# Performance work log

Measured on AMD Instinct MI355X. Metric: run time of the kernel, lower is better.

Reference implementation:

```python
import jax, jax.numpy as jnp
import numpy as np

B, SQ, SKV, D = 16, 4096, 4096, 64

def setup_inputs() -> dict:
    key = jax.random.key(0)
    kq, kk, kv, ks = jax.random.split(key, 4)
    return {
        "q": jax.random.normal(kq, (B, SQ, D), dtype=jnp.float32),
        "k": jax.random.normal(kk, (B, SKV, D), dtype=jnp.float32),
        "v": jax.random.normal(kv, (B, SKV, D), dtype=jnp.float32),
        "scale_factor": jax.random.uniform(ks, (1,), dtype=jnp.float32, minval=0.05, maxval=0.2),
    }

def reference(q, k, v, scale_factor):
    # qk = q @ k^T, then divide by inv_scale = 1/scale  ==  multiply by scale
    scores = jnp.einsum("bqd,bkd->bqk", q, k) * scale_factor[0]  # [B, SQ, SKV]
    probs = jax.nn.softmax(scores, axis=-1)
    # dropout p=0.0 -> identity (source's p=1 would zero the output; see notes)
    out = jnp.einsum("bqk,bkd->bqd", probs, v)  # [B, SQ, D]
    return out
```

## Files before the change

### kernel.cpp

```cpp
#include <hip/hip_runtime.h>
#include <hip/hip_bf16.h>

#define BATCH 16
#define SEQ   4096
#define DH    64
#define KVB   64
#define NT    (SEQ / KVB)
#define LDK   72

using frag   = __attribute__((ext_vector_type(8))) short;
using f32x16 = __attribute__((ext_vector_type(16))) float;
using u16x8  = __attribute__((ext_vector_type(8))) unsigned short;

__device__ __forceinline__ unsigned short f2bf(float x) {
    union { __hip_bfloat16 h; unsigned short u; } cv;
    cv.h = __float2bfloat16(x);
    return cv.u;
}
__device__ __forceinline__ unsigned int pk2bf(float lo, float hi) {
    return (unsigned int)f2bf(lo) | ((unsigned int)f2bf(hi) << 16);
}
__device__ __forceinline__ float fast_exp2(float x) {
#if __has_builtin(__builtin_amdgcn_exp2f)
    return __builtin_amdgcn_exp2f(x);
#else
    float r; asm("v_exp_f32 %0, %1" : "=v"(r) : "v"(x)); return r;
#endif
}
__device__ __forceinline__ unsigned int cvtpk_bf16(float lo, float hi) {
    unsigned int r;
    asm("v_cvt_pk_bf16_f32 %0, %1, %2" : "=v"(r) : "v"(lo), "v"(hi));
    return r;
}
__device__ __forceinline__ void glds16(const unsigned short* g, unsigned short* l) {
    __builtin_amdgcn_global_load_lds(
        (const __attribute__((address_space(1))) void*)g,
        (__attribute__((address_space(3))) void*)l, 16, 0, 0);
}

__global__ __launch_bounds__(256) void cvt_k_frag(const float* __restrict__ K,
                                                  unsigned short* __restrict__ Kws) {
    __shared__ unsigned short Ls[64 * LDK];
    const int b = blockIdx.x >> 6;
    const int t = blockIdx.x & 63;
    const int i = threadIdx.x;
    {
        const int kv = i >> 2, db = (i & 3) * 16;
        const float* src = K + ((size_t)b * SEQ + (size_t)t * 64 + kv) * DH + db;
        float4 a = *(const float4*)(src);
        float4 c = *(const float4*)(src + 4);
        float4 d = *(const float4*)(src + 8);
        float4 e = *(const float4*)(src + 12);
        u16x8 w0, w1;
        w0[0]=f2bf(a.x); w0[1]=f2bf(a.y); w0[2]=f2bf(a.z); w0[3]=f2bf(a.w);
        w0[4]=f2bf(c.x); w0[5]=f2bf(c.y); w0[6]=f2bf(c.z); w0[7]=f2bf(c.w);
        w1[0]=f2bf(d.x); w1[1]=f2bf(d.y); w1[2]=f2bf(d.z); w1[3]=f2bf(d.w);
        w1[4]=f2bf(e.x); w1[5]=f2bf(e.y); w1[6]=f2bf(e.z); w1[7]=f2bf(e.w);
        *(u16x8*)&Ls[kv * LDK + db]     = w0;
        *(u16x8*)&Ls[kv * LDK + db + 8] = w1;
    }
    __syncthreads();
    {
        const int flat0 = i * 2;
        const int f     = flat0 >> 6;
        const int kb    = f & 1, kstep = f >> 1;
        const int l0    = flat0 & 63, l1 = l0 + 1;
        u16x8 o0 = *(const u16x8*)&Ls[(kb*32 + (l0&31)) * LDK + kstep*16 + (l0>>5)*8];
        u16x8 o1 = *(const u16x8*)&Ls[(kb*32 + (l1&31)) * LDK + kstep*16 + (l1>>5)*8];
        unsigned short* dst = Kws + ((((size_t)b*64 + t)*8 + f)*64 + l0)*8;
        *(u16x8*)dst       = o0;
        *(u16x8*)(dst + 8) = o1;
    }
}

__global__ __launch_bounds__(256) void tr_v_frag(const float* __restrict__ V,
                                                 unsigned short* __restrict__ Vws) {
    __shared__ unsigned short Ls[64 * LDK];
    const int b = blockIdx.x >> 6;
    const int t = blockIdx.x & 63;
    const int i = threadIdx.x;
    {
        const int kv = i >> 2, db = (i & 3) * 16;
        const float* src = V + ((size_t)b * SEQ + (size_t)t * 64 + kv) * DH + db;
        float4 a = *(const float4*)(src);
        float4 c = *(const float4*)(src + 4);
        float4 d = *(const float4*)(src + 8);
        float4 e = *(const float4*)(src + 12);
        u16x8 w0, w1;
        w0[0]=f2bf(a.x); w0[1]=f2bf(a.y); w0[2]=f2bf(a.z); w0[3]=f2bf(a.w);
        w0[4]=f2bf(c.x); w0[5]=f2bf(c.y); w0[6]=f2bf(c.z); w0[7]=f2bf(c.w);
        w1[0]=f2bf(d.x); w1[1]=f2bf(d.y); w1[2]=f2bf(d.z); w1[3]=f2bf(d.w);
        w1[4]=f2bf(e.x); w1[5]=f2bf(e.y); w1[6]=f2bf(e.z); w1[7]=f2bf(e.w);
        *(u16x8*)&Ls[kv * LDK + db]     = w0;
        *(u16x8*)&Ls[kv * LDK + db + 8] = w1;
    }
    __syncthreads();
    {
        const int flat0 = i * 2;
        const int fv    = flat0 >> 6;
        const int kb    = fv >> 2, ks = (fv >> 1) & 1, dblk = fv & 1;
        u16x8 o0, o1;
        const int l0 = flat0 & 63, l1 = l0 + 1;
#pragma unroll
        for (int j = 0; j < 8; ++j)
            o0[j] = Ls[(kb*32 + ks*16 + (l0>>5)*8 + j) * LDK + dblk*32 + (l0&31)];
#pragma unroll
        for (int j = 0; j < 8; ++j)
            o1[j] = Ls[(kb*32 + ks*16 + (l1>>5)*8 + j) * LDK + dblk*32 + (l1&31)];
        unsigned short* dst = Vws + ((((size_t)b*64 + t)*8 + fv)*64 + l0)*8;
        *(u16x8*)dst       = o0;
        *(u16x8*)(dst + 8) = o1;
    }
}

__global__ __launch_bounds__(128, 2) void attn_fwd(
    const float* __restrict__ Q, const unsigned short* __restrict__ Kws,
    const unsigned short* __restrict__ Vws, const float* __restrict__ S,
    float* __restrict__ O)
{
    __shared__ unsigned short Kbuf[2][8 * 64 * 8];
    __shared__ unsigned short Vbuf[2][8 * 64 * 8];

    const int bid   = blockIdx.x;
    const int xcd   = bid & 7;
    const int sub   = bid >> 3;
    const int batch = xcd + ((sub & 1) << 3);
    const int qtile = sub >> 1;

    const int tid  = threadIdx.x;
    const int w    = tid >> 6;
    const int lane = tid & 63;
    const int c32  = lane & 31;
    const int hi   = lane >> 5;

    const float sc = S[0] * 1.44269504088896340736f;

    const float*          Qb = Q   + ((size_t)batch * SEQ + (size_t)qtile * 64 + w * 32) * DH;
    const unsigned short* Kg = Kws + (size_t)batch * 64 * 8 * 512;
    const unsigned short* Vg = Vws + (size_t)batch * 64 * 8 * 512;

    frag qF[4];
#pragma unroll
    for (int kstep = 0; kstep < 4; ++kstep) {
        const float* p = Qb + c32 * DH + kstep * 16 + hi * 8;
        float4 a = *(const float4*)p;
        float4 b = *(const float4*)(p + 4);
        frag f;
        f[0] = (short)f2bf(a.x * sc); f[1] = (short)f2bf(a.y * sc);
        f[2] = (short)f2bf(a.z * sc); f[3] = (short)f2bf(a.w * sc);
        f[4] = (short)f2bf(b.x * sc); f[5] = (short)f2bf(b.y * sc);
        f[6] = (short)f2bf(b.z * sc); f[7] = (short)f2bf(b.w * sc);
        qF[kstep] = f;
    }

    frag ones;
#pragma unroll
    for (int j = 0; j < 8; ++j) ones[j] = (short)0x3F80;

    f32x16 o32[2];
    f32x16 l32;
    o32[0] = (f32x16)0.0f; o32[1] = (f32x16)0.0f; l32 = (f32x16)0.0f;

    const unsigned short* gsrc = (w == 0) ? Kg : Vg;
#pragma unroll
    for (int f = 0; f < 8; ++f) {
        unsigned short* lp = (w == 0) ? &Kbuf[0][f * 512] : &Vbuf[0][f * 512];
        glds16(gsrc + (size_t)0 * 4096 + f * 512 + lane * 8, lp);
    }
    asm volatile("s_waitcnt vmcnt(0)" ::: "memory");
    __builtin_amdgcn_s_barrier();
    __builtin_amdgcn_sched_barrier(0);

    for (int t = 0; t < NT; ++t) {
        const int cur = t & 1;
        if (t + 1 < NT) {
#pragma unroll
            for (int f = 0; f < 8; ++f) {
                unsigned short* lp = (w == 0) ? &Kbuf[cur ^ 1][f * 512] : &Vbuf[cur ^ 1][f * 512];
                glds16(gsrc + (size_t)(t + 1) * 4096 + f * 512 + lane * 8, lp);
            }
        }

        f32x16 st[2];
        st[0] = (f32x16)0.0f; st[1] = (f32x16)0.0f;
        __builtin_amdgcn_s_setprio(1);
#pragma unroll
        for (int kstep = 0; kstep < 4; ++kstep)
#pragma unroll
          for (int kb = 0; kb < 2; ++kb) {
            frag kf = *(const frag*)&Kbuf[cur][(kstep * 2 + kb) * 512 + lane * 8];
            st[kb] = __builtin_amdgcn_mfma_f32_32x32x16_bf16(kf, qF[kstep], st[kb], 0, 0, 0);
          }
        __builtin_amdgcn_s_setprio(0);

        frag pa[2][2];
#pragma unroll
        for (int kb = 0; kb < 2; ++kb) {
            float p[16];
#pragma unroll
            for (int r = 0; r < 16; ++r) p[r] = fast_exp2(st[kb][r]);
            unsigned a0 = cvtpk_bf16(p[0],  p[1]),  a1 = cvtpk_bf16(p[2],  p[3]);
            unsigned b0 = cvtpk_bf16(p[4],  p[5]),  b1 = cvtpk_bf16(p[6],  p[7]);
            unsigned c0 = cvtpk_bf16(p[8],  p[9]),  c1 = cvtpk_bf16(p[10], p[11]);
            unsigned d0 = cvtpk_bf16(p[12], p[13]), d1 = cvtpk_bf16(p[14], p[15]);
            asm("v_permlane32_swap_b32 %0, %1" : "+v"(a0), "+v"(b0));
            asm("v_permlane32_swap_b32 %0, %1" : "+v"(a1), "+v"(b1));
            asm("v_permlane32_swap_b32 %0, %1" : "+v"(c0), "+v"(d0));
            asm("v_permlane32_swap_b32 %0, %1" : "+v"(c1), "+v"(d1));
            union { unsigned u[4]; frag f; } f0, f1;
            f0.u[0] = a0; f0.u[1] = a1; f0.u[2] = b0; f0.u[3] = b1;
            f1.u[0] = c0; f1.u[1] = c1; f1.u[2] = d0; f1.u[3] = d1;
            pa[kb][0] = f0.f;
            pa[kb][1] = f1.f;
        }

        __builtin_amdgcn_s_setprio(1);
#pragma unroll
        for (int kb = 0; kb < 2; ++kb)
#pragma unroll
          for (int ks = 0; ks < 2; ++ks) {
            l32 = __builtin_amdgcn_mfma_f32_32x32x16_bf16(pa[kb][ks], ones, l32, 0, 0, 0);
#pragma unroll
            for (int dblk = 0; dblk < 2; ++dblk) {
                frag vf = *(const frag*)&Vbuf[cur][((kb * 2 + ks) * 2 + dblk) * 512 + lane * 8];
                o32[dblk] = __builtin_amdgcn_mfma_f32_32x32x16_bf16(pa[kb][ks], vf, o32[dblk], 0, 0, 0);
            }
          }
        __builtin_amdgcn_s_setprio(0);

        asm volatile("s_waitcnt vmcnt(0)" ::: "memory");
        __builtin_amdgcn_s_barrier();
        __builtin_amdgcn_sched_barrier(0);
    }

    float* Ob = O + ((size_t)batch * SEQ + (size_t)qtile * 64 + w * 32) * DH;
    float inv[16];
#pragma unroll
    for (int r = 0; r < 16; ++r) inv[r] = 1.0f / l32[r];
#pragma unroll
    for (int dblk = 0; dblk < 2; ++dblk)
#pragma unroll
      for (int r = 0; r < 16; ++r) {
        const int qrow = (r & 3) + 8 * (r >> 2) + 4 * hi;
        Ob[qrow * DH + dblk * 32 + c32] = o32[dblk][r] * inv[r];
      }
}

extern "C" void kernel_launch(void* const* d_in, const int* in_sizes, int n_in,
                              void* d_out, int out_size, void* d_ws, size_t ws_size,
                              hipStream_t stream) {
    const float* q = (const float*)d_in[0];
    const float* k = (const float*)d_in[1];
    const float* v = (const float*)d_in[2];
    const float* s = (const float*)d_in[3];
    float* o = (float*)d_out;

    unsigned short* kws = (unsigned short*)d_ws;
    unsigned short* vws = kws + (size_t)BATCH * SEQ * DH;

    cvt_k_frag<<<dim3(BATCH * 64), dim3(256), 0, stream>>>(k, kws);
    tr_v_frag <<<dim3(BATCH * 64), dim3(256), 0, stream>>>(v, vws);

    const int blocks = BATCH * (SEQ / 64);
    attn_fwd<<<dim3(blocks), dim3(128), 0, stream>>>(q, kws, vws, s, o);
}
```

Measured before the change: 105.2 us.

## Software-pipeline QK^T one tile ahead and split K/V loads across both waves

Restructures the attention loop so the QK^T MFMAs for tile t+1 are issued in the same iteration as the exp/PV work for tile t. K is prefetched two tiles ahead and V one tile ahead, with ping-pong buffers and the loop unrolled by two. Each wave now loads half of both K and V instead of one wave loading all of K and the other all of V. The aim is to overlap the MFMA pipes with the softmax ALU work and balance load issue, at the cost of extra live score registers, which may pressure occupancy.

Result: no change. 105.8 us (+0.6%).

```diff
diff --git a/kernel.cpp b/kernel.cpp
--- a/kernel.cpp
+++ b/kernel.cpp
@@ -17,9 +17,6 @@
     cv.h = __float2bfloat16(x);
     return cv.u;
 }
-__device__ __forceinline__ unsigned int pk2bf(float lo, float hi) {
-    return (unsigned int)f2bf(lo) | ((unsigned int)f2bf(hi) << 16);
-}
 __device__ __forceinline__ float fast_exp2(float x) {
 #if __has_builtin(__builtin_amdgcn_exp2f)
     return __builtin_amdgcn_exp2f(x);
@@ -36,6 +33,9 @@
     __builtin_amdgcn_global_load_lds(
         (const __attribute__((address_space(1))) void*)g,
         (__attribute__((address_space(3))) void*)l, 16, 0, 0);
+}
+__device__ __forceinline__ f32x16 mfma32(frag a, frag b, f32x16 c) {
+    return __builtin_amdgcn_mfma_f32_32x32x16_bf16(a, b, c, 0, 0, 0);
 }
 
 __global__ __launch_bounds__(256) void cvt_k_frag(const float* __restrict__ K,
@@ -118,8 +118,8 @@
     const unsigned short* __restrict__ Vws, const float* __restrict__ S,
     float* __restrict__ O)
 {
-    __shared__ unsigned short Kbuf[2][8 * 64 * 8];
-    __shared__ unsigned short Vbuf[2][8 * 64 * 8];
+    __shared__ unsigned short Kb0[8 * 64 * 8], Kb1[8 * 64 * 8];
+    __shared__ unsigned short Vb0[8 * 64 * 8], Vb1[8 * 64 * 8];
 
     const int bid   = blockIdx.x;
     const int xcd   = bid & 7;
@@ -161,44 +161,68 @@
     f32x16 l32;
     o32[0] = (f32x16)0.0f; o32[1] = (f32x16)0.0f; l32 = (f32x16)0.0f;
 
-    const unsigned short* gsrc = (w == 0) ? Kg : Vg;
-#pragma unroll
-    for (int f = 0; f < 8; ++f) {
-        unsigned short* lp = (w == 0) ? &Kbuf[0][f * 512] : &Vbuf[0][f * 512];
-        glds16(gsrc + (size_t)0 * 4096 + f * 512 + lane * 8, lp);
+    f32x16 stA[2], stB[2];
+
+    const int fbase = w * 4;
+
+#pragma unroll
+    for (int f = 0; f < 4; ++f) {
+        glds16(Kg + (size_t)0 * 4096 + (fbase + f) * 512 + lane * 8, Kb0 + (fbase + f) * 512);
+        glds16(Vg + (size_t)0 * 4096 + (fbase + f) * 512 + lane * 8, Vb0 + (fbase + f) * 512);
+        glds16(Kg + (size_t)1 * 4096 + (fbase + f) * 512 + lane * 8, Kb1 + (fbase + f) * 512);
     }
     asm volatile("s_waitcnt vmcnt(0)" ::: "memory");
     __builtin_amdgcn_s_barrier();
     __builtin_amdgcn_sched_barrier(0);
 
-    for (int t = 0; t < NT; ++t) {
-        const int cur = t & 1;
+    stA[0] = (f32x16)0.0f; stA[1] = (f32x16)0.0f;
+#pragma unroll
+    for (int kstep = 0; kstep < 4; ++kstep)
+#pragma unroll
+      for (int kb = 0; kb < 2; ++kb) {
+        frag kf = *(const frag*)(Kb0 + (kstep * 2 + kb) * 512 + lane * 8);
+        stA[kb] = mfma32(kf, qF[kstep], stA[kb]);
+      }
+
+    auto body = [&](int t, unsigned short* KbWr, unsigned short* VbWr,
+                    const unsigned short* KbRd, const unsigned short* VbRd,
+                    f32x16 (&stIn)[2], f32x16 (&stOut)[2]) __attribute__((always_inline)) {
+        asm volatile("s_waitcnt vmcnt(0)" ::: "memory");
+        __builtin_amdgcn_s_barrier();
+        __builtin_amdgcn_sched_barrier(0);
+
+        if (t + 2 < NT) {
+#pragma unroll
+            for (int f = 0; f < 4; ++f)
+                glds16(Kg + (size_t)(t + 2) * 4096 + (fbase + f) * 512 + lane * 8,
+                       KbWr + (fbase + f) * 512);
+        }
         if (t + 1 < NT) {
 #pragma unroll
-            for (int f = 0; f < 8; ++f) {
-                unsigned short* lp = (w == 0) ? &Kbuf[cur ^ 1][f * 512] : &Vbuf[cur ^ 1][f * 512];
-                glds16(gsrc + (size_t)(t + 1) * 4096 + f * 512 + lane * 8, lp);
-            }
-        }
-
-        f32x16 st[2];
-        st[0] = (f32x16)0.0f; st[1] = (f32x16)0.0f;
-        __builtin_amdgcn_s_setprio(1);
-#pragma unroll
-        for (int kstep = 0; kstep < 4; ++kstep)
-#pragma unroll
-          for (int kb = 0; kb < 2; ++kb) {
-            frag kf = *(const frag*)&Kbuf[cur][(kstep * 2 + kb) * 512 + lane * 8];
-            st[kb] = __builtin_amdgcn_mfma_f32_32x32x16_bf16(kf, qF[kstep], st[kb], 0, 0, 0);
-          }
-        __builtin_amdgcn_s_setprio(0);
+            for (int f = 0; f < 4; ++f)
+                glds16(Vg + (size_t)(t + 1) * 4096 + (fbase + f) * 512 + lane * 8,
+                       VbWr + (fbase + f) * 512);
+        }
+
+        if (t + 1 < NT) {
+            stOut[0] = (f32x16)0.0f; stOut[1] = (f32x16)0.0f;
+            __builtin_amdgcn_s_setprio(1);
+#pragma unroll
+            for (int kstep = 0; kstep < 4; ++kstep)
+#pragma unroll
+              for (int kb = 0; kb < 2; ++kb) {
+                frag kf = *(const frag*)(KbRd + (kstep * 2 + kb) * 512 + lane * 8);
+                stOut[kb] = mfma32(kf, qF[kstep], stOut[kb]);
+              }
+            __builtin_amdgcn_s_setprio(0);
+        }
 
         frag pa[2][2];
 #pragma unroll
         for (int kb = 0; kb < 2; ++kb) {
             float p[16];
 #pragma unroll
-            for (int r = 0; r < 16; ++r) p[r] = fast_exp2(st[kb][r]);
+            for (int r = 0; r < 16; ++r) p[r] = fast_exp2(stIn[kb][r]);
             unsigned a0 = cvtpk_bf16(p[0],  p[1]),  a1 = cvtpk_bf16(p[2],  p[3]);
             unsigned b0 = cvtpk_bf16(p[4],  p[5]),  b1 = cvtpk_bf16(p[6],  p[7]);
             unsigned c0 = cvtpk_bf16(p[8],  p[9]),  c1 = cvtpk_bf16(p[10], p[11]);
@@ -219,18 +243,19 @@
         for (int kb = 0; kb < 2; ++kb)
 #pragma unroll
           for (int ks = 0; ks < 2; ++ks) {
-            l32 = __builtin_amdgcn_mfma_f32_32x32x16_bf16(pa[kb][ks], ones, l32, 0, 0, 0);
+            l32 = mfma32(pa[kb][ks], ones, l32);
 #pragma unroll
             for (int dblk = 0; dblk < 2; ++dblk) {
-                frag vf = *(const frag*)&Vbuf[cur][((kb * 2 + ks) * 2 + dblk) * 512 + lane * 8];
-                o32[dblk] = __builtin_amdgcn_mfma_f32_32x32x16_bf16(pa[kb][ks], vf, o32[dblk], 0, 0, 0);
+                frag vf = *(const frag*)(VbRd + ((kb * 2 + ks) * 2 + dblk) * 512 + lane * 8);
+                o32[dblk] = mfma32(pa[kb][ks], vf, o32[dblk]);
             }
           }
         __builtin_amdgcn_s_setprio(0);
-
-        asm volatile("s_waitcnt vmcnt(0)" ::: "memory");
-        __builtin_amdgcn_s_barrier();
-        __builtin_amdgcn_sched_barrier(0);
+    };
+
+    for (int t = 0; t < NT; t += 2) {
+        body(t,     Kb0, Vb1, Kb1, Vb0, stA, stB);
+        body(t + 1, Kb1, Vb0, Kb0, Vb1, stB, stA);
     }
 
     float* Ob = O + ((size_t)batch * SEQ + (size_t)qtile * 64 + w * 32) * DH;
```

## Use 4-wave blocks over 128 query rows and split KV range in two

Applied to the files above, without the earlier changes.

Blocks grow from 2 to 4 waves, each block covering 128 query rows, and K/V tile loads are spread across all four waves. When workspace allows, the KV sequence is split into two halves handled by separate blocks. Each half writes unnormalized partial outputs and row sums, and a new merge kernel adds them and normalizes. This raises K/V reuse per LDS tile and the number of concurrent blocks, in exchange for an extra kernel launch and extra global traffic for the partial outputs. The split is valid without max rescaling because the kernel never subtracts a running max.

New measurement: 103.5 us. About the same (-1.6%).

```diff
diff --git a/kernel.cpp b/kernel.cpp
--- a/kernel.cpp
+++ b/kernel.cpp
@@ -17,9 +17,6 @@
     cv.h = __float2bfloat16(x);
     return cv.u;
 }
-__device__ __forceinline__ unsigned int pk2bf(float lo, float hi) {
-    return (unsigned int)f2bf(lo) | ((unsigned int)f2bf(hi) << 16);
-}
 __device__ __forceinline__ float fast_exp2(float x) {
 #if __has_builtin(__builtin_amdgcn_exp2f)
     return __builtin_amdgcn_exp2f(x);
@@ -36,6 +33,9 @@
     __builtin_amdgcn_global_load_lds(
         (const __attribute__((address_space(1))) void*)g,
         (__attribute__((address_space(3))) void*)l, 16, 0, 0);
+}
+__device__ __forceinline__ f32x16 mfma32(frag a, frag b, f32x16 c) {
+    return __builtin_amdgcn_mfma_f32_32x32x16_bf16(a, b, c, 0, 0, 0);
 }
 
 __global__ __launch_bounds__(256) void cvt_k_frag(const float* __restrict__ K,
@@ -113,19 +113,22 @@
     }
 }
 
-__global__ __launch_bounds__(128, 2) void attn_fwd(
+__global__ __launch_bounds__(256, 4) void attn_fwd(
     const float* __restrict__ Q, const unsigned short* __restrict__ Kws,
     const unsigned short* __restrict__ Vws, const float* __restrict__ S,
-    float* __restrict__ O)
+    float* __restrict__ O0, float* __restrict__ O1,
+    float* __restrict__ l0p, float* __restrict__ l1p, int nsplit)
 {
     __shared__ unsigned short Kbuf[2][8 * 64 * 8];
     __shared__ unsigned short Vbuf[2][8 * 64 * 8];
 
-    const int bid   = blockIdx.x;
-    const int xcd   = bid & 7;
-    const int sub   = bid >> 3;
-    const int batch = xcd + ((sub & 1) << 3);
-    const int qtile = sub >> 1;
+    const int bid = blockIdx.x;
+    const int xcd = bid & 7;
+    int sub = bid >> 3;
+    int half = 0;
+    if (nsplit == 2) { half = sub & 1; sub >>= 1; }
+    const int batch = xcd | ((sub & 1) << 3);
+    const int qt    = sub >> 1;
 
     const int tid  = threadIdx.x;
     const int w    = tid >> 6;
@@ -133,9 +136,12 @@
     const int c32  = lane & 31;
     const int hi   = lane >> 5;
 
+    const int t0   = half * (NT / 2);
+    const int ntil = NT / nsplit;
+
     const float sc = S[0] * 1.44269504088896340736f;
 
-    const float*          Qb = Q   + ((size_t)batch * SEQ + (size_t)qtile * 64 + w * 32) * DH;
+    const float*          Qb = Q   + ((size_t)batch * SEQ + (size_t)qt * 128 + w * 32) * DH;
     const unsigned short* Kg = Kws + (size_t)batch * 64 * 8 * 512;
     const unsigned short* Vg = Vws + (size_t)batch * 64 * 8 * 512;
 
@@ -161,23 +167,26 @@
     f32x16 l32;
     o32[0] = (f32x16)0.0f; o32[1] = (f32x16)0.0f; l32 = (f32x16)0.0f;
 
-    const unsigned short* gsrc = (w == 0) ? Kg : Vg;
-#pragma unroll
-    for (int f = 0; f < 8; ++f) {
-        unsigned short* lp = (w == 0) ? &Kbuf[0][f * 512] : &Vbuf[0][f * 512];
-        glds16(gsrc + (size_t)0 * 4096 + f * 512 + lane * 8, lp);
+    const int fbase = w * 2;
+#pragma unroll
+    for (int f = 0; f < 2; ++f) {
+        glds16(Kg + (size_t)t0 * 4096 + (fbase + f) * 512 + lane * 8, &Kbuf[0][(fbase + f) * 512]);
+        glds16(Vg + (size_t)t0 * 4096 + (fbase + f) * 512 + lane * 8, &Vbuf[0][(fbase + f) * 512]);
     }
     asm volatile("s_waitcnt vmcnt(0)" ::: "memory");
     __builtin_amdgcn_s_barrier();
     __builtin_amdgcn_sched_barrier(0);
 
-    for (int t = 0; t < NT; ++t) {
-        const int cur = t & 1;
-        if (t + 1 < NT) {
-#pragma unroll
-            for (int f = 0; f < 8; ++f) {
-                unsigned short* lp = (w == 0) ? &Kbuf[cur ^ 1][f * 512] : &Vbuf[cur ^ 1][f * 512];
-                glds16(gsrc + (size_t)(t + 1) * 4096 + f * 512 + lane * 8, lp);
+    for (int tt = 0; tt < ntil; ++tt) {
+        const int t   = t0 + tt;
+        const int cur = tt & 1;
+        if (tt + 1 < ntil) {
+#pragma unroll
+            for (int f = 0; f < 2; ++f) {
+                glds16(Kg + (size_t)(t + 1) * 4096 + (fbase + f) * 512 + lane * 8,
+                       &Kbuf[cur ^ 1][(fbase + f) * 512]);
+                glds16(Vg + (size_t)(t + 1) * 4096 + (fbase + f) * 512 + lane * 8,
+                       &Vbuf[cur ^ 1][(fbase + f) * 512]);
             }
         }
 
@@ -189,7 +198,7 @@
 #pragma unroll
           for (int kb = 0; kb < 2; ++kb) {
             frag kf = *(const frag*)&Kbuf[cur][(kstep * 2 + kb) * 512 + lane * 8];
-            st[kb] = __builtin_amdgcn_mfma_f32_32x32x16_bf16(kf, qF[kstep], st[kb], 0, 0, 0);
+            st[kb] = mfma32(kf, qF[kstep], st[kb]);
           }
         __builtin_amdgcn_s_setprio(0);
 
@@ -219,11 +228,11 @@
         for (int kb = 0; kb < 2; ++kb)
 #pragma unroll
           for (int ks = 0; ks < 2; ++ks) {
-            l32 = __builtin_amdgcn_mfma_f32_32x32x16_bf16(pa[kb][ks], ones, l32, 0, 0, 0);
+            l32 = mfma32(pa[kb][ks], ones, l32);
 #pragma unroll
             for (int dblk = 0; dblk < 2; ++dblk) {
                 frag vf = *(const frag*)&Vbuf[cur][((kb * 2 + ks) * 2 + dblk) * 512 + lane * 8];
-                o32[dblk] = __builtin_amdgcn_mfma_f32_32x32x16_bf16(pa[kb][ks], vf, o32[dblk], 0, 0, 0);
+                o32[dblk] = mfma32(pa[kb][ks], vf, o32[dblk]);
             }
           }
         __builtin_amdgcn_s_setprio(0);
@@ -233,17 +242,55 @@
         __builtin_amdgcn_sched_barrier(0);
     }
 
-    float* Ob = O + ((size_t)batch * SEQ + (size_t)qtile * 64 + w * 32) * DH;
-    float inv[16];
-#pragma unroll
-    for (int r = 0; r < 16; ++r) inv[r] = 1.0f / l32[r];
-#pragma unroll
-    for (int dblk = 0; dblk < 2; ++dblk)
-#pragma unroll
-      for (int r = 0; r < 16; ++r) {
-        const int qrow = (r & 3) + 8 * (r >> 2) + 4 * hi;
-        Ob[qrow * DH + dblk * 32 + c32] = o32[dblk][r] * inv[r];
-      }
+    const size_t qrow0 = (size_t)batch * SEQ + (size_t)qt * 128 + w * 32;
+    if (nsplit == 1) {
+        float* Ob = O0 + qrow0 * DH;
+        float inv[16];
+#pragma unroll
+        for (int r = 0; r < 16; ++r) inv[r] = 1.0f / l32[r];
+#pragma unroll
+        for (int dblk = 0; dblk < 2; ++dblk)
+#pragma unroll
+          for (int r = 0; r < 16; ++r) {
+            const int qrow = (r & 3) + 8 * (r >> 2) + 4 * hi;
+            Ob[qrow * DH + dblk * 32 + c32] = o32[dblk][r] * inv[r];
+          }
+    } else {
+        float* Ob = (half ? O1 : O0) + qrow0 * DH;
+        float* lb = (half ? l1p : l0p) + qrow0;
+#pragma unroll
+        for (int dblk = 0; dblk < 2; ++dblk)
+#pragma unroll
+          for (int r = 0; r < 16; ++r) {
+            const int qrow = (r & 3) + 8 * (r >> 2) + 4 * hi;
+            Ob[qrow * DH + dblk * 32 + c32] = o32[dblk][r];
+          }
+        if (c32 == 0) {
+#pragma unroll
+            for (int r = 0; r < 16; ++r) {
+                const int qrow = (r & 3) + 8 * (r >> 2) + 4 * hi;
+                lb[qrow] = l32[r];
+            }
+        }
+    }
+}
+
+__global__ __launch_bounds__(256) void merge_halves(
+    float* __restrict__ O, const float* __restrict__ O1,
+    const float* __restrict__ l0, const float* __restrict__ l1)
+{
+    const size_t i0  = ((size_t)blockIdx.x * 256 + threadIdx.x) * 8;
+    const size_t row = i0 >> 6;
+    const float inv  = 1.0f / (l0[row] + l1[row]);
+    float4 a0 = *(const float4*)(O  + i0), a1 = *(const float4*)(O  + i0 + 4);
+    float4 b0 = *(const float4*)(O1 + i0), b1 = *(const float4*)(O1 + i0 + 4);
+    float4 r0, r1;
+    r0.x = (a0.x + b0.x) * inv; r0.y = (a0.y + b0.y) * inv;
+    r0.z = (a0.z + b0.z) * inv; r0.w = (a0.w + b0.w) * inv;
+    r1.x = (a1.x + b1.x) * inv; r1.y = (a1.y + b1.y) * inv;
+    r1.z = (a1.z + b1.z) * inv; r1.w = (a1.w + b1.w) * inv;
+    *(float4*)(O + i0)     = r0;
+    *(float4*)(O + i0 + 4) = r1;
 }
 
 extern "C" void kernel_launch(void* const* d_in, const int* in_sizes, int n_in,
@@ -255,12 +302,21 @@
     const float* s = (const float*)d_in[3];
     float* o = (float*)d_out;
 
+    const size_t kv_elems = (size_t)BATCH * SEQ * DH;
     unsigned short* kws = (unsigned short*)d_ws;
-    unsigned short* vws = kws + (size_t)BATCH * SEQ * DH;
+    unsigned short* vws = kws + kv_elems;
+    float* o1 = (float*)(vws + kv_elems);
+    float* l0 = o1 + kv_elems;
+    float* l1 = l0 + (size_t)BATCH * SEQ;
+    const size_t need = kv_elems * 2 * 2 + kv_elems * 4 + (size_t)BATCH * SEQ * 8;
 
     cvt_k_frag<<<dim3(BATCH * 64), dim3(256), 0, stream>>>(k, kws);
     tr_v_frag <<<dim3(BATCH * 64), dim3(256), 0, stream>>>(v, vws);
 
-    const int blocks = BATCH * (SEQ / 64);
-    attn_fwd<<<dim3(blocks), dim3(128), 0, stream>>>(q, kws, vws, s, o);
-}
+    if (ws_size >= need) {
+        attn_fwd<<<dim3(1024), dim3(256), 0, stream>>>(q, kws, vws, s, o, o1, l0, l1, 2);
+        merge_halves<<<dim3((BATCH * SEQ * DH) / (256 * 8)), dim3(256), 0, stream>>>(o, o1, l0, l1);
+    } else {
+        attn_fwd<<<dim3(512), dim3(256), 0, stream>>>(q, kws, vws, s, o, nullptr, nullptr, nullptr, 1);
+    }
+}
```
